# Kernel optimization log

Hardware: AMD Instinct MI355X
Metric: run time of the kernel (lower is better)

## Reference

```python
import jax, jax.numpy as jnp
import numpy as np

B, H, N, DK, DV = 2, 8, 2048, 64, 64

def setup_inputs() -> dict:
    key = jax.random.key(0)
    k1, k2, k3, k4 = jax.random.split(key, 4)
    q = jax.random.normal(k1, (B, H, N, DK), dtype=jnp.float32)
    k = jax.random.normal(k2, (B, H, N, DK), dtype=jnp.float32)
    v = jax.random.normal(k3, (B, H, N, DV), dtype=jnp.float32)
    # decay mask, strictly positive in (0,1)
    omask = jax.random.uniform(k4, (B, H, N, N), dtype=jnp.float32, minval=1e-3, maxval=1.0)
    return {"q": q, "k": k, "v": v, "omask": omask}

def reference(q, k, v, omask):
    # coefficients from the decay mask
    q_bar_coef = omask[..., :, 0] / jnp.sqrt(omask.sum(axis=-1))  # (B,H,n)
    k_bar_coef = 1.0 / omask[..., :, 0]                            # (B,H,n)
    q_bar = q_bar_coef[..., None] * q                               # (B,H,n,dk)
    k_bar = k_bar_coef[..., None] * k                               # (B,H,n,dk)
    # normalizer P (detached in original)
    T = jnp.cumsum(k_bar, axis=-2)                                  # (B,H,n,dk)
    P = jnp.einsum('bhia,bhia->bhi', T, q_bar)                      # (B,H,n)
    P = jnp.maximum(jnp.abs(jax.lax.stop_gradient(P)), 1.0)[..., None]
    # cumulative outer-product state D: (B,H,n,dk,dv)
    D = jnp.cumsum(jnp.einsum('bhia,bhic->bhiac', k_bar, v), axis=-3)
    O = jnp.einsum('bhia,bhiac->bhic', q_bar, D) / P                # (B,H,n,dv)
    return O
```

## Files before the change

### kernel.cpp

```cpp
#include <hip/hip_runtime.h>
#include <cmath>

constexpr int B_ = 2, H_ = 8, N_ = 2048, DK_ = 64, DV_ = 64;
constexpr int BH_ = B_ * H_;
constexpr int C_ = 64;
constexpr int NC_ = N_ / C_;
constexpr int NCH_ = BH_ * NC_;

using f32x16 = __attribute__((ext_vector_type(16))) float;
using bf16x8 = __attribute__((ext_vector_type(8))) __bf16;

__device__ inline unsigned short bfr(float x) {
  unsigned u = __float_as_uint(x);
  return (unsigned short)((u + 0x7FFFu + ((u >> 16) & 1u)) >> 16);
}
__device__ inline unsigned pk2(float lo, float hi) {
  return (unsigned)bfr(lo) | ((unsigned)bfr(hi) << 16);
}
__device__ inline int swi(int row, int a) {
  return (row * 128 + (((a * 2) ^ ((row & 7) << 4)))) >> 1;
}

__global__ __launch_bounds__(256) void coef_kernel(const float* __restrict__ om,
                                                   float* __restrict__ qc,
                                                   float* __restrict__ kc) {
  int row = blockIdx.x * 4 + (threadIdx.x >> 6);
  int lane = threadIdx.x & 63;
  const float* r = om + (size_t)row * N_;
  float s = 0.f;
#pragma unroll
  for (int kk = 0; kk < N_ / 256; ++kk) {
    float4 v4 = *(const float4*)(r + kk * 256 + lane * 4);
    s += (v4.x + v4.y) + (v4.z + v4.w);
  }
#pragma unroll
  for (int off = 32; off > 0; off >>= 1) s += __shfl_xor(s, off, 64);
  if (lane == 0) {
    float o0 = r[0];
    qc[row] = o0 / sqrtf(s);
    kc[row] = 1.0f / o0;
  }
}

__global__ __launch_bounds__(256) void chunksum_kernel(const float* __restrict__ kg,
                                                       const float* __restrict__ vg,
                                                       const float* __restrict__ kc,
                                                       float* __restrict__ ksum,
                                                       float* __restrict__ kvsum) {
  __shared__ float kb[C_][DK_];
  __shared__ float vs[C_][DV_];
  int chunk = blockIdx.x;
  int bh = chunk / NC_, ci = chunk - bh * NC_;
  int r0 = ci * C_;
  size_t gbase = ((size_t)bh * N_ + r0) * DK_;
  int t = threadIdx.x;
#pragma unroll
  for (int p = 0; p < 4; ++p) {
    int f = t + p * 256;
    int row = f >> 4, col = (f & 15) * 4;
    float sc = kc[bh * N_ + r0 + row];
    float4 k4 = *(const float4*)(kg + gbase + (size_t)f * 4);
    k4.x *= sc; k4.y *= sc; k4.z *= sc; k4.w *= sc;
    *(float4*)&kb[row][col] = k4;
    *(float4*)&vs[row][col] = *(const float4*)(vg + gbase + (size_t)f * 4);
  }
  __syncthreads();
  int dk0 = (t & 15) * 4, dv0 = (t >> 4) * 4;
  float acc[4][4] = {};
  float ks[4] = {};
  for (int r = 0; r < C_; ++r) {
    float4 k4 = *(const float4*)&kb[r][dk0];
    float4 v4 = *(const float4*)&vs[r][dv0];
    float ka[4] = {k4.x, k4.y, k4.z, k4.w};
    float va[4] = {v4.x, v4.y, v4.z, v4.w};
#pragma unroll
    for (int i = 0; i < 4; ++i) {
      ks[i] += ka[i];
#pragma unroll
      for (int j = 0; j < 4; ++j) acc[i][j] += ka[i] * va[j];
    }
  }
  float* kvc = kvsum + (size_t)chunk * (DK_ * DV_);
#pragma unroll
  for (int i = 0; i < 4; ++i)
    *(float4*)(kvc + (size_t)(dk0 + i) * DV_ + dv0) =
        make_float4(acc[i][0], acc[i][1], acc[i][2], acc[i][3]);
  if (t < 16) {
#pragma unroll
    for (int i = 0; i < 4; ++i) ksum[(size_t)chunk * DK_ + dk0 + i] = ks[i];
  }
}

__global__ __launch_bounds__(256) void scan_kernel(float* __restrict__ ksum,
                                                   float* __restrict__ kvsum) {
  constexpr int PER = DK_ * DV_ + DK_;
  int idx = blockIdx.x * 256 + threadIdx.x;
  if (idx >= BH_ * PER) return;
  int bh = idx / PER, e = idx - bh * PER;
  float run = 0.f;
  if (e < DK_ * DV_) {
    float* p = kvsum + (size_t)bh * NC_ * (DK_ * DV_) + e;
    for (int ci = 0; ci < NC_; ++ci) {
      float tv = p[(size_t)ci * (DK_ * DV_)];
      p[(size_t)ci * (DK_ * DV_)] = run;
      run += tv;
    }
  } else {
    float* p = ksum + (size_t)bh * NC_ * DK_ + (e - DK_ * DV_);
    for (int ci = 0; ci < NC_; ++ci) {
      float tv = p[(size_t)ci * DK_];
      p[(size_t)ci * DK_] = run;
      run += tv;
    }
  }
}

__global__ __launch_bounds__(256) void out_mfma_kernel(
    const float* __restrict__ qg, const float* __restrict__ kg,
    const float* __restrict__ vg, const float* __restrict__ qc,
    const float* __restrict__ kc, const float* __restrict__ ksum,
    const float* __restrict__ kvsum, float* __restrict__ outg) {
  __shared__ unsigned short qb[64 * 64];
  __shared__ unsigned short kb[64 * 64];
  __shared__ unsigned short sS[64 * 64];
  __shared__ unsigned short vT[64 * 64];
  __shared__ unsigned short dT[64 * 64];
  __shared__ float Tc[2][64][68];
  __shared__ float Tl[64];
  __shared__ float Pf[64];

  const int chunk = blockIdx.x;
  const int bh = chunk >> 5, ci = chunk & 31;
  const int r0 = ci * C_;
  const int rowb = bh * N_ + r0;
  const size_t gbase = (size_t)rowb * DK_;
  const int t = threadIdx.x;
  const int i = t >> 2, a0 = (t & 3) * 16;

  float xq[16];
  {
    float qcv = qc[rowb + i];
    float kcv = kc[rowb + i];
    float xk[16], xv[16], xd[16];
    {
      const float* qp = qg + gbase + (size_t)i * 64 + a0;
      const float* kp = kg + gbase + (size_t)i * 64 + a0;
      const float* vp = vg + gbase + (size_t)i * 64 + a0;
      const float* dp = kvsum + (size_t)chunk * (DK_ * DV_) + (size_t)i * 64 + a0;
#pragma unroll
      for (int u = 0; u < 4; ++u) {
        *(float4*)&xq[u * 4] = *(const float4*)(qp + u * 4);
        *(float4*)&xk[u * 4] = *(const float4*)(kp + u * 4);
        *(float4*)&xv[u * 4] = *(const float4*)(vp + u * 4);
        *(float4*)&xd[u * 4] = *(const float4*)(dp + u * 4);
      }
    }
#pragma unroll
    for (int u = 0; u < 16; ++u) { xq[u] *= qcv; xk[u] *= kcv; }
#pragma unroll
    for (int u4 = 0; u4 < 4; ++u4)
      *(float4*)&Tc[0][i][a0 + u4 * 4] = *(const float4*)&xk[u4 * 4];
    unsigned* qbu = (unsigned*)qb;
    unsigned* kbu = (unsigned*)kb;
#pragma unroll
    for (int u = 0; u < 8; ++u) {
      int a = a0 + 2 * u;
      int bi = (i * 128 + (((a * 2) ^ ((i & 7) << 4)))) >> 2;
      qbu[bi] = pk2(xq[2 * u], xq[2 * u + 1]);
      kbu[bi] = pk2(xk[2 * u], xk[2 * u + 1]);
    }
#pragma unroll
    for (int u = 0; u < 16; ++u) {
      int c = a0 + u;
      vT[swi(c, i)] = bfr(xv[u]);
      dT[swi(c, i)] = bfr(xd[u]);
    }
    if (t < 64) Tl[t] = ksum[(size_t)chunk * DK_ + t];
  }
  __syncthreads();

  {
    int p = 0;
#pragma unroll
    for (int step = 1; step < 64; step <<= 1) {
      float4 cur[4], prv[4];
#pragma unroll
      for (int u4 = 0; u4 < 4; ++u4) {
        cur[u4] = *(const float4*)&Tc[p][i][a0 + u4 * 4];
        if (i >= step)
          prv[u4] = *(const float4*)&Tc[p][i - step][a0 + u4 * 4];
        else
          prv[u4] = make_float4(0.f, 0.f, 0.f, 0.f);
      }
#pragma unroll
      for (int u4 = 0; u4 < 4; ++u4) {
        float4 w = make_float4(cur[u4].x + prv[u4].x, cur[u4].y + prv[u4].y,
                               cur[u4].z + prv[u4].z, cur[u4].w + prv[u4].w);
        *(float4*)&Tc[p ^ 1][i][a0 + u4 * 4] = w;
      }
      __syncthreads();
      p ^= 1;
    }
  }

  {
    float part = 0.f;
#pragma unroll
    for (int u = 0; u < 16; ++u)
      part += xq[u] * (Tl[a0 + u] + Tc[0][i][a0 + u]);
    part += __shfl_xor(part, 1, 64);
    part += __shfl_xor(part, 2, 64);
    if ((t & 3) == 0) Pf[i] = 1.0f / fmaxf(fabsf(part), 1.0f);
  }

  const int lane = t & 63, w = t >> 6;
  const int wr = w >> 1, wc = w & 1;
  const int half = lane >> 5, col = lane & 31;
  const int arow = 32 * wr + col;
  const int bcol = 32 * wc + col;

  f32x16 accS;
#pragma unroll
  for (int r = 0; r < 16; ++r) accS[r] = 0.f;
#pragma unroll
  for (int kk = 0; kk < 4; ++kk) {
    int aa = kk * 16 + half * 8;
    bf16x8 af = *(const bf16x8*)&qb[swi(arow, aa)];
    bf16x8 bf = *(const bf16x8*)&kb[swi(bcol, aa)];
    accS = __builtin_amdgcn_mfma_f32_32x32x16_bf16(af, bf, accS, 0, 0, 0);
  }
#pragma unroll
  for (int r = 0; r < 16; ++r) {
    int iloc = (r & 3) + 8 * (r >> 2) + 4 * half;
    int ii = 32 * wr + iloc;
    int jj = 32 * wc + col;
    float m = (jj <= ii) ? accS[r] : 0.f;
    sS[swi(ii, jj)] = bfr(m);
  }
  __syncthreads();

  f32x16 acc;
#pragma unroll
  for (int r = 0; r < 16; ++r) acc[r] = 0.f;
#pragma unroll
  for (int kk = 0; kk < 4; ++kk) {
    int j0 = kk * 16 + half * 8;
    bf16x8 af = *(const bf16x8*)&sS[swi(arow, j0)];
    bf16x8 bf = *(const bf16x8*)&vT[swi(bcol, j0)];
    acc = __builtin_amdgcn_mfma_f32_32x32x16_bf16(af, bf, acc, 0, 0, 0);
  }
#pragma unroll
  for (int kk = 0; kk < 4; ++kk) {
    int aa = kk * 16 + half * 8;
    bf16x8 af = *(const bf16x8*)&qb[swi(arow, aa)];
    bf16x8 bf = *(const bf16x8*)&dT[swi(bcol, aa)];
    acc = __builtin_amdgcn_mfma_f32_32x32x16_bf16(af, bf, acc, 0, 0, 0);
  }

  float* ob = outg + (size_t)rowb * DV_;
#pragma unroll
  for (int r = 0; r < 16; ++r) {
    int iloc = (r & 3) + 8 * (r >> 2) + 4 * half;
    int ii = 32 * wr + iloc;
    int cc = 32 * wc + col;
    ob[(size_t)ii * DV_ + cc] = acc[r] * Pf[ii];
  }
}

extern "C" void kernel_launch(void* const* d_in, const int* in_sizes, int n_in,
                              void* d_out, int out_size, void* d_ws, size_t ws_size,
                              hipStream_t stream) {
  const float* q = (const float*)d_in[0];
  const float* k = (const float*)d_in[1];
  const float* v = (const float*)d_in[2];
  const float* om = (const float*)d_in[3];
  float* out = (float*)d_out;

  float* ws = (float*)d_ws;
  float* qc = ws;
  float* kc = qc + BH_ * N_;
  float* ksum = kc + BH_ * N_;
  float* kv = ksum + (size_t)NCH_ * DK_;

  coef_kernel<<<BH_ * N_ / 4, 256, 0, stream>>>(om, qc, kc);
  chunksum_kernel<<<NCH_, 256, 0, stream>>>(k, v, kc, ksum, kv);
  constexpr int SCAN_TOTAL = BH_ * (DK_ * DV_ + DK_);
  scan_kernel<<<(SCAN_TOTAL + 255) / 256, 256, 0, stream>>>(ksum, kv);
  out_mfma_kernel<<<NCH_, 256, 0, stream>>>(q, k, v, qc, kc, ksum, kv, out);
}
```

Measured before the change: 68.06 us.

## Fuse chunk-sum, scan and output kernels into one cooperative kernel with grid syncs

Replaces the chunksum, scan and output launches with a single cooperative kernel. Each block loads q/k/v once, computes its chunk's kv outer-product sum and in-chunk k prefix, then grid-syncs. Blocks then run a float4-vectorized cross-chunk exclusive scan, grid-sync again, and compute the output with MFMA. This removes two launches and redundant reloads of k/v, at the cost of two grid-wide barriers and the scan running on only a fraction of threads. It falls back to the old three-kernel path if the cooperative launch fails.

```diff
diff --git a/kernel.cpp b/kernel.cpp
--- a/kernel.cpp
+++ b/kernel.cpp
@@ -1,5 +1,8 @@
 #include <hip/hip_runtime.h>
+#include <hip/hip_cooperative_groups.h>
 #include <cmath>
+
+namespace cg = cooperative_groups;
 
 constexpr int B_ = 2, H_ = 8, N_ = 2048, DK_ = 64, DV_ = 64;
 constexpr int BH_ = B_ * H_;
@@ -42,12 +45,231 @@
   }
 }
 
+__global__ __launch_bounds__(256, 2) void fused_tail(
+    const float* __restrict__ qg, const float* __restrict__ kg,
+    const float* __restrict__ vg, const float* __restrict__ qc,
+    const float* __restrict__ kc, float* __restrict__ lksum,
+    float* __restrict__ lkv, float* __restrict__ outg) {
+  __shared__ float Tc[2][64][68];
+  __shared__ unsigned short qb[64 * 64];
+  __shared__ unsigned short kb[64 * 64];
+  __shared__ unsigned short vT[64 * 64];
+  __shared__ float poolv[64 * 64];
+  __shared__ float Tl[64];
+  __shared__ float Pf[64];
+
+  const int chunk = blockIdx.x;
+  const int bh = chunk >> 5, ci = chunk & 31;
+  const int r0 = ci * C_;
+  const int rowb = bh * N_ + r0;
+  const size_t gbase = (size_t)rowb * DK_;
+  const int t = threadIdx.x;
+  const int i = t >> 2, a0 = (t & 3) * 16;
+
+  float xq[16];
+
+  {
+    float qcv = qc[rowb + i];
+    float kcv = kc[rowb + i];
+    float xk[16], xv[16];
+    {
+      const float* qp = qg + gbase + (size_t)i * 64 + a0;
+      const float* kp = kg + gbase + (size_t)i * 64 + a0;
+      const float* vp = vg + gbase + (size_t)i * 64 + a0;
+#pragma unroll
+      for (int u = 0; u < 4; ++u) {
+        *(float4*)&xq[u * 4] = *(const float4*)(qp + u * 4);
+        *(float4*)&xk[u * 4] = *(const float4*)(kp + u * 4);
+        *(float4*)&xv[u * 4] = *(const float4*)(vp + u * 4);
+      }
+    }
+#pragma unroll
+    for (int u = 0; u < 16; ++u) { xq[u] *= qcv; xk[u] *= kcv; }
+#pragma unroll
+    for (int u4 = 0; u4 < 4; ++u4) {
+      *(float4*)&Tc[0][i][a0 + u4 * 4] = *(const float4*)&xk[u4 * 4];
+      *(float4*)&poolv[i * 64 + a0 + u4 * 4] = *(const float4*)&xv[u4 * 4];
+    }
+    unsigned* qbu = (unsigned*)qb;
+    unsigned* kbu = (unsigned*)kb;
+#pragma unroll
+    for (int u = 0; u < 8; ++u) {
+      int a = a0 + 2 * u;
+      int bi = (i * 128 + (((a * 2) ^ ((i & 7) << 4)))) >> 2;
+      qbu[bi] = pk2(xq[2 * u], xq[2 * u + 1]);
+      kbu[bi] = pk2(xk[2 * u], xk[2 * u + 1]);
+    }
+#pragma unroll
+    for (int u = 0; u < 16; ++u) vT[swi(a0 + u, i)] = bfr(xv[u]);
+  }
+  __syncthreads();
+
+  {
+    int dk0 = (t & 15) * 4, dv0 = (t >> 4) * 4;
+    float acc[4][4] = {};
+    for (int r = 0; r < C_; ++r) {
+      float4 k4 = *(const float4*)&Tc[0][r][dk0];
+      float4 v4 = *(const float4*)&poolv[r * 64 + dv0];
+      float ka[4] = {k4.x, k4.y, k4.z, k4.w};
+      float va[4] = {v4.x, v4.y, v4.z, v4.w};
+#pragma unroll
+      for (int ii = 0; ii < 4; ++ii)
+#pragma unroll
+        for (int jj = 0; jj < 4; ++jj) acc[ii][jj] += ka[ii] * va[jj];
+    }
+    float* kvc = lkv + (size_t)chunk * (DK_ * DV_);
+#pragma unroll
+    for (int ii = 0; ii < 4; ++ii)
+      *(float4*)(kvc + (size_t)(dk0 + ii) * DV_ + dv0) =
+          make_float4(acc[ii][0], acc[ii][1], acc[ii][2], acc[ii][3]);
+  }
+  __syncthreads();
+
+  {
+    int p = 0;
+#pragma unroll
+    for (int step = 1; step < 64; step <<= 1) {
+      float4 cur[4], prv[4];
+#pragma unroll
+      for (int u4 = 0; u4 < 4; ++u4) {
+        cur[u4] = *(const float4*)&Tc[p][i][a0 + u4 * 4];
+        if (i >= step)
+          prv[u4] = *(const float4*)&Tc[p][i - step][a0 + u4 * 4];
+        else
+          prv[u4] = make_float4(0.f, 0.f, 0.f, 0.f);
+      }
+#pragma unroll
+      for (int u4 = 0; u4 < 4; ++u4) {
+        float4 w = make_float4(cur[u4].x + prv[u4].x, cur[u4].y + prv[u4].y,
+                               cur[u4].z + prv[u4].z, cur[u4].w + prv[u4].w);
+        *(float4*)&Tc[p ^ 1][i][a0 + u4 * 4] = w;
+      }
+      __syncthreads();
+      p ^= 1;
+    }
+  }
+  if (i == 63) {
+#pragma unroll
+    for (int u = 0; u < 16; ++u)
+      lksum[(size_t)chunk * DK_ + a0 + u] = Tc[0][63][a0 + u];
+  }
+
+  cg::this_grid().sync();
+
+  {
+    constexpr int PER4 = (DK_ * DV_) / 4 + DK_ / 4;
+    int tid = blockIdx.x * 256 + t;
+    if (tid < BH_ * PER4) {
+      int sbh = tid / PER4, e = tid - sbh * PER4;
+      float4* p;
+      size_t stride;
+      if (e < (DK_ * DV_) / 4) {
+        p = (float4*)(lkv + (size_t)sbh * NC_ * (DK_ * DV_)) + e;
+        stride = (DK_ * DV_) / 4;
+      } else {
+        p = (float4*)(lksum + (size_t)sbh * NC_ * DK_) + (e - (DK_ * DV_) / 4);
+        stride = DK_ / 4;
+      }
+      float4 run = make_float4(0.f, 0.f, 0.f, 0.f);
+      float4 buf[8];
+      for (int b = 0; b < NC_ / 8; ++b) {
+#pragma unroll
+        for (int u = 0; u < 8; ++u) buf[u] = p[(size_t)(b * 8 + u) * stride];
+#pragma unroll
+        for (int u = 0; u < 8; ++u) {
+          p[(size_t)(b * 8 + u) * stride] = run;
+          run.x += buf[u].x; run.y += buf[u].y;
+          run.z += buf[u].z; run.w += buf[u].w;
+        }
+      }
+    }
+  }
+
+  cg::this_grid().sync();
+
+  unsigned short* dT = (unsigned short*)poolv;
+  unsigned short* sS = (unsigned short*)(poolv + 2048);
+  {
+    const float* dp = lkv + (size_t)chunk * (DK_ * DV_) + (size_t)i * 64 + a0;
+    float xd[16];
+#pragma unroll
+    for (int u = 0; u < 4; ++u) *(float4*)&xd[u * 4] = *(const float4*)(dp + u * 4);
+#pragma unroll
+    for (int u = 0; u < 16; ++u) dT[swi(a0 + u, i)] = bfr(xd[u]);
+    if (t < 64) Tl[t] = lksum[(size_t)chunk * DK_ + t];
+  }
+  __syncthreads();
+
+  {
+    float part = 0.f;
+#pragma unroll
+    for (int u = 0; u < 16; ++u)
+      part += xq[u] * (Tl[a0 + u] + Tc[0][i][a0 + u]);
+    part += __shfl_xor(part, 1, 64);
+    part += __shfl_xor(part, 2, 64);
+    if ((t & 3) == 0) Pf[i] = 1.0f / fmaxf(fabsf(part), 1.0f);
+  }
+
+  const int lane = t & 63, w = t >> 6;
+  const int wr = w >> 1, wc = w & 1;
+  const int half = lane >> 5, col = lane & 31;
+  const int arow = 32 * wr + col;
+  const int bcol = 32 * wc + col;
+
+  f32x16 accS;
+#pragma unroll
+  for (int r = 0; r < 16; ++r) accS[r] = 0.f;
+#pragma unroll
+  for (int kk = 0; kk < 4; ++kk) {
+    int aa = kk * 16 + half * 8;
+    bf16x8 af = *(const bf16x8*)&qb[swi(arow, aa)];
+    bf16x8 bf = *(const bf16x8*)&kb[swi(bcol, aa)];
+    accS = __builtin_amdgcn_mfma_f32_32x32x16_bf16(af, bf, accS, 0, 0, 0);
+  }
+#pragma unroll
+  for (int r = 0; r < 16; ++r) {
+    int iloc = (r & 3) + 8 * (r >> 2) + 4 * half;
+    int ii = 32 * wr + iloc;
+    int jj = 32 * wc + col;
+    float m = (jj <= ii) ? accS[r] : 0.f;
+    sS[swi(ii, jj)] = bfr(m);
+  }
+  __syncthreads();
+
+  f32x16 acc;
+#pragma unroll
+  for (int r = 0; r < 16; ++r) acc[r] = 0.f;
+#pragma unroll
+  for (int kk = 0; kk < 4; ++kk) {
+    int j0 = kk * 16 + half * 8;
+    bf16x8 af = *(const bf16x8*)&sS[swi(arow, j0)];
+    bf16x8 bf = *(const bf16x8*)&vT[swi(bcol, j0)];
+    acc = __builtin_amdgcn_mfma_f32_32x32x16_bf16(af, bf, acc, 0, 0, 0);
+  }
+#pragma unroll
+  for (int kk = 0; kk < 4; ++kk) {
+    int aa = kk * 16 + half * 8;
+    bf16x8 af = *(const bf16x8*)&qb[swi(arow, aa)];
+    bf16x8 bf = *(const bf16x8*)&dT[swi(bcol, aa)];
+    acc = __builtin_amdgcn_mfma_f32_32x32x16_bf16(af, bf, acc, 0, 0, 0);
+  }
+
+  float* ob = outg + (size_t)rowb * DV_;
+#pragma unroll
+  for (int r = 0; r < 16; ++r) {
+    int iloc = (r & 3) + 8 * (r >> 2) + 4 * half;
+    int ii = 32 * wr + iloc;
+    int cc = 32 * wc + col;
+    ob[(size_t)ii * DV_ + cc] = acc[r] * Pf[ii];
+  }
+}
+
 __global__ __launch_bounds__(256) void chunksum_kernel(const float* __restrict__ kg,
                                                        const float* __restrict__ vg,
                                                        const float* __restrict__ kc,
                                                        float* __restrict__ ksum,
                                                        float* __restrict__ kvsum) {
-  __shared__ float kb[C_][DK_];
+  __shared__ float kbf[C_][DK_];
   __shared__ float vs[C_][DV_];
   int chunk = blockIdx.x;
   int bh = chunk / NC_, ci = chunk - bh * NC_;
@@ -61,7 +283,7 @@
     float sc = kc[bh * N_ + r0 + row];
     float4 k4 = *(const float4*)(kg + gbase + (size_t)f * 4);
     k4.x *= sc; k4.y *= sc; k4.z *= sc; k4.w *= sc;
-    *(float4*)&kb[row][col] = k4;
+    *(float4*)&kbf[row][col] = k4;
     *(float4*)&vs[row][col] = *(const float4*)(vg + gbase + (size_t)f * 4);
   }
   __syncthreads();
@@ -69,25 +291,25 @@
   float acc[4][4] = {};
   float ks[4] = {};
   for (int r = 0; r < C_; ++r) {
-    float4 k4 = *(const float4*)&kb[r][dk0];
+    float4 k4 = *(const float4*)&kbf[r][dk0];
     float4 v4 = *(const float4*)&vs[r][dv0];
     float ka[4] = {k4.x, k4.y, k4.z, k4.w};
     float va[4] = {v4.x, v4.y, v4.z, v4.w};
 #pragma unroll
-    for (int i = 0; i < 4; ++i) {
-      ks[i] += ka[i];
-#pragma unroll
-      for (int j = 0; j < 4; ++j) acc[i][j] += ka[i] * va[j];
+    for (int ii = 0; ii < 4; ++ii) {
+      ks[ii] += ka[ii];
+#pragma unroll
+      for (int jj = 0; jj < 4; ++jj) acc[ii][jj] += ka[ii] * va[jj];
     }
   }
   float* kvc = kvsum + (size_t)chunk * (DK_ * DV_);
 #pragma unroll
-  for (int i = 0; i < 4; ++i)
-    *(float4*)(kvc + (size_t)(dk0 + i) * DV_ + dv0) =
-        make_float4(acc[i][0], acc[i][1], acc[i][2], acc[i][3]);
+  for (int ii = 0; ii < 4; ++ii)
+    *(float4*)(kvc + (size_t)(dk0 + ii) * DV_ + dv0) =
+        make_float4(acc[ii][0], acc[ii][1], acc[ii][2], acc[ii][3]);
   if (t < 16) {
 #pragma unroll
-    for (int i = 0; i < 4; ++i) ksum[(size_t)chunk * DK_ + dk0 + i] = ks[i];
+    for (int ii = 0; ii < 4; ++ii) ksum[(size_t)chunk * DK_ + dk0 + ii] = ks[ii];
   }
 }
 
@@ -178,7 +400,6 @@
     if (t < 64) Tl[t] = ksum[(size_t)chunk * DK_ + t];
   }
   __syncthreads();
-
   {
     int p = 0;
 #pragma unroll
@@ -202,7 +423,6 @@
       p ^= 1;
     }
   }
-
   {
     float part = 0.f;
 #pragma unroll
@@ -212,13 +432,11 @@
     part += __shfl_xor(part, 2, 64);
     if ((t & 3) == 0) Pf[i] = 1.0f / fmaxf(fabsf(part), 1.0f);
   }
-
   const int lane = t & 63, w = t >> 6;
   const int wr = w >> 1, wc = w & 1;
   const int half = lane >> 5, col = lane & 31;
   const int arow = 32 * wr + col;
   const int bcol = 32 * wc + col;
-
   f32x16 accS;
 #pragma unroll
   for (int r = 0; r < 16; ++r) accS[r] = 0.f;
@@ -238,7 +456,6 @@
     sS[swi(ii, jj)] = bfr(m);
   }
   __syncthreads();
-
   f32x16 acc;
 #pragma unroll
   for (int r = 0; r < 16; ++r) acc[r] = 0.f;
@@ -256,7 +473,6 @@
     bf16x8 bf = *(const bf16x8*)&dT[swi(bcol, aa)];
     acc = __builtin_amdgcn_mfma_f32_32x32x16_bf16(af, bf, acc, 0, 0, 0);
   }
-
   float* ob = outg + (size_t)rowb * DV_;
 #pragma unroll
   for (int r = 0; r < 16; ++r) {
@@ -283,8 +499,15 @@
   float* kv = ksum + (size_t)NCH_ * DK_;
 
   coef_kernel<<<BH_ * N_ / 4, 256, 0, stream>>>(om, qc, kc);
-  chunksum_kernel<<<NCH_, 256, 0, stream>>>(k, v, kc, ksum, kv);
-  constexpr int SCAN_TOTAL = BH_ * (DK_ * DV_ + DK_);
-  scan_kernel<<<(SCAN_TOTAL + 255) / 256, 256, 0, stream>>>(ksum, kv);
-  out_mfma_kernel<<<NCH_, 256, 0, stream>>>(q, k, v, qc, kc, ksum, kv, out);
-}
+
+  void* args[] = {(void*)&q, (void*)&k, (void*)&v, (void*)&qc, (void*)&kc,
+                  (void*)&ksum, (void*)&kv, (void*)&out};
+  hipError_t err = hipLaunchCooperativeKernel((void*)fused_tail, dim3(NCH_),
+                                              dim3(256), args, 0, stream);
+  if (err != hipSuccess) {
+    chunksum_kernel<<<NCH_, 256, 0, stream>>>(k, v, kc, ksum, kv);
+    constexpr int SCAN_TOTAL = BH_ * (DK_ * DV_ + DK_);
+    scan_kernel<<<(SCAN_TOTAL + 255) / 256, 256, 0, stream>>>(ksum, kv);
+    out_mfma_kernel<<<NCH_, 256, 0, stream>>>(q, k, v, qc, kc, ksum, kv, out);
+  }
+}
```

Result: slower. 191.6 us (+181.5%).

## Fuse coefficient reduction into scan kernel and compute k coef in chunksum

Applied to the files above, without the earlier changes.

The chunksum kernel now computes 1/omask[i,0] itself, so it no longer waits on the coefficient kernel. The omask row-sum reduction is merged into the scan kernel as extra blocks, so the bandwidth-heavy reduction runs alongside the chunk-prefix scan in one launch. The scan is also vectorised to float4 with batched loads of 8 chunks. This removes one launch and one serial dependency, at the cost of a strided gather of omask's first column in chunksum and a heterogeneous grid.

```diff
diff --git a/kernel.cpp b/kernel.cpp
--- a/kernel.cpp
+++ b/kernel.cpp
@@ -6,6 +6,7 @@
 constexpr int C_ = 64;
 constexpr int NC_ = N_ / C_;
 constexpr int NCH_ = BH_ * NC_;
+constexpr int SCAN_BLOCKS = (BH_ * ((DK_ * DV_) / 4 + DK_ / 4)) / 256;
 
 using f32x16 = __attribute__((ext_vector_type(16))) float;
 using bf16x8 = __attribute__((ext_vector_type(8))) __bf16;
@@ -21,44 +22,27 @@
   return (row * 128 + (((a * 2) ^ ((row & 7) << 4)))) >> 1;
 }
 
-__global__ __launch_bounds__(256) void coef_kernel(const float* __restrict__ om,
-                                                   float* __restrict__ qc,
-                                                   float* __restrict__ kc) {
-  int row = blockIdx.x * 4 + (threadIdx.x >> 6);
-  int lane = threadIdx.x & 63;
-  const float* r = om + (size_t)row * N_;
-  float s = 0.f;
-#pragma unroll
-  for (int kk = 0; kk < N_ / 256; ++kk) {
-    float4 v4 = *(const float4*)(r + kk * 256 + lane * 4);
-    s += (v4.x + v4.y) + (v4.z + v4.w);
-  }
-#pragma unroll
-  for (int off = 32; off > 0; off >>= 1) s += __shfl_xor(s, off, 64);
-  if (lane == 0) {
-    float o0 = r[0];
-    qc[row] = o0 / sqrtf(s);
-    kc[row] = 1.0f / o0;
-  }
-}
-
 __global__ __launch_bounds__(256) void chunksum_kernel(const float* __restrict__ kg,
                                                        const float* __restrict__ vg,
-                                                       const float* __restrict__ kc,
+                                                       const float* __restrict__ om,
                                                        float* __restrict__ ksum,
                                                        float* __restrict__ kvsum) {
   __shared__ float kb[C_][DK_];
   __shared__ float vs[C_][DV_];
+  __shared__ float smkc[C_];
   int chunk = blockIdx.x;
   int bh = chunk / NC_, ci = chunk - bh * NC_;
   int r0 = ci * C_;
-  size_t gbase = ((size_t)bh * N_ + r0) * DK_;
+  int rowb = bh * N_ + r0;
+  size_t gbase = (size_t)rowb * DK_;
   int t = threadIdx.x;
+  if (t < 64) smkc[t] = 1.0f / om[(size_t)(rowb + t) * N_];
+  __syncthreads();
 #pragma unroll
   for (int p = 0; p < 4; ++p) {
     int f = t + p * 256;
     int row = f >> 4, col = (f & 15) * 4;
-    float sc = kc[bh * N_ + r0 + row];
+    float sc = smkc[row];
     float4 k4 = *(const float4*)(kg + gbase + (size_t)f * 4);
     k4.x *= sc; k4.y *= sc; k4.z *= sc; k4.w *= sc;
     *(float4*)&kb[row][col] = k4;
@@ -91,26 +75,53 @@
   }
 }
 
-__global__ __launch_bounds__(256) void scan_kernel(float* __restrict__ ksum,
-                                                   float* __restrict__ kvsum) {
-  constexpr int PER = DK_ * DV_ + DK_;
-  int idx = blockIdx.x * 256 + threadIdx.x;
-  if (idx >= BH_ * PER) return;
-  int bh = idx / PER, e = idx - bh * PER;
-  float run = 0.f;
-  if (e < DK_ * DV_) {
-    float* p = kvsum + (size_t)bh * NC_ * (DK_ * DV_) + e;
-    for (int ci = 0; ci < NC_; ++ci) {
-      float tv = p[(size_t)ci * (DK_ * DV_)];
-      p[(size_t)ci * (DK_ * DV_)] = run;
-      run += tv;
+__global__ __launch_bounds__(256) void coef_scan_kernel(const float* __restrict__ om,
+                                                        float* __restrict__ qc,
+                                                        float* __restrict__ kc,
+                                                        float* __restrict__ ksum,
+                                                        float* __restrict__ kvsum) {
+  int t = threadIdx.x;
+  if (blockIdx.x < SCAN_BLOCKS) {
+    constexpr int PER4 = (DK_ * DV_) / 4 + DK_ / 4;
+    int idx = blockIdx.x * 256 + t;
+    int bh = idx / PER4, e = idx - bh * PER4;
+    float4* p;
+    size_t stride;
+    if (e < (DK_ * DV_) / 4) {
+      p = (float4*)(kvsum + (size_t)bh * NC_ * (DK_ * DV_)) + e;
+      stride = (DK_ * DV_) / 4;
+    } else {
+      p = (float4*)(ksum + (size_t)bh * NC_ * DK_) + (e - (DK_ * DV_) / 4);
+      stride = DK_ / 4;
+    }
+    float4 run = make_float4(0.f, 0.f, 0.f, 0.f);
+    float4 buf[8];
+    for (int b = 0; b < NC_ / 8; ++b) {
+#pragma unroll
+      for (int u = 0; u < 8; ++u) buf[u] = p[(size_t)(b * 8 + u) * stride];
+#pragma unroll
+      for (int u = 0; u < 8; ++u) {
+        p[(size_t)(b * 8 + u) * stride] = run;
+        run.x += buf[u].x; run.y += buf[u].y;
+        run.z += buf[u].z; run.w += buf[u].w;
+      }
     }
   } else {
-    float* p = ksum + (size_t)bh * NC_ * DK_ + (e - DK_ * DV_);
-    for (int ci = 0; ci < NC_; ++ci) {
-      float tv = p[(size_t)ci * DK_];
-      p[(size_t)ci * DK_] = run;
-      run += tv;
+    int row = (blockIdx.x - SCAN_BLOCKS) * 4 + (t >> 6);
+    int lane = t & 63;
+    const float* r = om + (size_t)row * N_;
+    float s = 0.f;
+#pragma unroll
+    for (int kk = 0; kk < N_ / 256; ++kk) {
+      float4 v4 = *(const float4*)(r + kk * 256 + lane * 4);
+      s += (v4.x + v4.y) + (v4.z + v4.w);
+    }
+#pragma unroll
+    for (int off = 32; off > 0; off >>= 1) s += __shfl_xor(s, off, 64);
+    if (lane == 0) {
+      float o0 = r[0];
+      qc[row] = o0 / sqrtf(s);
+      kc[row] = 1.0f / o0;
     }
   }
 }
@@ -178,7 +189,6 @@
     if (t < 64) Tl[t] = ksum[(size_t)chunk * DK_ + t];
   }
   __syncthreads();
-
   {
     int p = 0;
 #pragma unroll
@@ -202,7 +212,6 @@
       p ^= 1;
     }
   }
-
   {
     float part = 0.f;
 #pragma unroll
@@ -212,13 +221,11 @@
     part += __shfl_xor(part, 2, 64);
     if ((t & 3) == 0) Pf[i] = 1.0f / fmaxf(fabsf(part), 1.0f);
   }
-
   const int lane = t & 63, w = t >> 6;
   const int wr = w >> 1, wc = w & 1;
   const int half = lane >> 5, col = lane & 31;
   const int arow = 32 * wr + col;
   const int bcol = 32 * wc + col;
-
   f32x16 accS;
 #pragma unroll
   for (int r = 0; r < 16; ++r) accS[r] = 0.f;
@@ -238,7 +245,6 @@
     sS[swi(ii, jj)] = bfr(m);
   }
   __syncthreads();
-
   f32x16 acc;
 #pragma unroll
   for (int r = 0; r < 16; ++r) acc[r] = 0.f;
@@ -256,7 +262,6 @@
     bf16x8 bf = *(const bf16x8*)&dT[swi(bcol, aa)];
     acc = __builtin_amdgcn_mfma_f32_32x32x16_bf16(af, bf, acc, 0, 0, 0);
   }
-
   float* ob = outg + (size_t)rowb * DV_;
 #pragma unroll
   for (int r = 0; r < 16; ++r) {
@@ -282,9 +287,8 @@
   float* ksum = kc + BH_ * N_;
   float* kv = ksum + (size_t)NCH_ * DK_;
 
-  coef_kernel<<<BH_ * N_ / 4, 256, 0, stream>>>(om, qc, kc);
-  chunksum_kernel<<<NCH_, 256, 0, stream>>>(k, v, kc, ksum, kv);
-  constexpr int SCAN_TOTAL = BH_ * (DK_ * DV_ + DK_);
-  scan_kernel<<<(SCAN_TOTAL + 255) / 256, 256, 0, stream>>>(ksum, kv);
+  chunksum_kernel<<<NCH_, 256, 0, stream>>>(k, v, om, ksum, kv);
+  coef_scan_kernel<<<SCAN_BLOCKS + BH_ * N_ / 4, 256, 0, stream>>>(om, qc, kc,
+                                                                   ksum, kv);
   out_mfma_kernel<<<NCH_, 256, 0, stream>>>(q, k, v, qc, kc, ksum, kv, out);
 }
```

After: 69.01 us. Within noise of the previous version (+1.4%).
